# Performance work log

Measured on AMD Instinct MI355X. Metric: run time of the kernel, lower is better.

Reference implementation:

```python
import jax, jax.numpy as jnp
import numpy as np
from jax import lax

B, N, C = 32, 4096, 512
HEADS, K, U = 4, 16, 4
V = C // HEADS  # 128
KS = 7
EPS = 1e-3  # keras LayerNormalization default epsilon


def _layernorm(x, g, b):
    mu = jnp.mean(x, axis=-1, keepdims=True)
    var = jnp.var(x, axis=-1, keepdims=True)
    return (x - mu) * lax.rsqrt(var + EPS) * g + b


def setup_inputs() -> dict:
    key = jax.random.key(0)
    ks = jax.random.split(key, 6)
    sc = lambda fan: 1.0 / np.sqrt(fan)
    x = jax.random.normal(ks[0], (B, N, C), dtype=jnp.float32)
    wq = jax.random.normal(ks[1], (C, K * HEADS), dtype=jnp.float32) * sc(C)
    wk = jax.random.normal(ks[2], (C, K * U), dtype=jnp.float32) * sc(C)
    wv = jax.random.normal(ks[3], (C, V * U), dtype=jnp.float32) * sc(C)
    gq = jnp.ones((K * HEADS,), jnp.float32)
    bq = jnp.zeros((K * HEADS,), jnp.float32)
    gv = jnp.ones((V * U,), jnp.float32)
    bv = jnp.zeros((V * U,), jnp.float32)
    pos_w = jax.random.normal(ks[4], (1, KS, U, K), dtype=jnp.float32) * sc(KS * U)
    pos_b = jnp.zeros((K,), jnp.float32)
    return {"x": x, "wq": wq, "wk": wk, "wv": wv, "gq": gq, "bq": bq,
            "gv": gv, "bv": bv, "pos_w": pos_w, "pos_b": pos_b}


def reference(x, wq, wk, wv, gq, bq, gv, bv, pos_w, pos_b):
    # 1x1 conv projections == per-position matmuls
    q = _layernorm(x @ wq, gq, bq)                      # (B, N, K*HEADS)
    k = x @ wk                                          # (B, N, K*U)
    v = _layernorm(x @ wv, gv, bv)                      # (B, N, V*U)
    # rearranges (Reshape + Permute((2,3,1)))
    q = q.reshape(B, N, HEADS, K).transpose(0, 2, 3, 1)  # (B, H, K, N)
    k = k.reshape(B, N, U, K).transpose(0, 2, 3, 1)      # (B, U, K, N)
    v = v.reshape(B, N, U, V).transpose(0, 2, 3, 1)      # (B, U, V, N)
    k = jax.nn.softmax(k, axis=-1)                       # softmax over positions n
    # content lambda
    lc = jnp.einsum('bukn,buvn->bkv', k, v)              # (B, K, V)
    yc = jnp.einsum('bhkn,bkv->bnhv', q, lc)             # (B, N, H, V)
    # positional lambda: Conv2D(K, (1, KS), 'same') over (B, V, N, U) NHWC
    v2 = v.transpose(0, 2, 3, 1)                         # (B, V, N, U)
    lp = lax.conv_general_dilated(v2, pos_w, (1, 1), 'SAME',
                                  dimension_numbers=('NHWC', 'HWIO', 'NHWC')) + pos_b  # (B, V, N, K)
    lp = lp.transpose(0, 1, 3, 2)                        # (B, V, K, N)
    yp = jnp.einsum('bhkn,bvkn->bnhv', q, lp)            # (B, N, H, V)
    return (yc + yp).reshape(B, N, HEADS * V)            # (B, N, out_dim)
```

## Files before the change

### kernel.cpp

```cpp
#include <hip/hip_runtime.h>
#include <hip/hip_bf16.h>


#define Bb   32
#define Nn   4096
#define Cc   512
#define Hh   4
#define Kk   16
#define Uu   4
#define Vv   128
#define QKVW 640
#define EPSf 1e-3f

typedef __bf16 bf16;
typedef bf16  bf16x8 __attribute__((ext_vector_type(8)));
typedef bf16  bf16x4 __attribute__((ext_vector_type(4)));
typedef float f32x4  __attribute__((ext_vector_type(4)));

#define WT_OFF   0UL
#define QKV_OFF  655360UL
#define QMU_OFF  168427520UL
#define QRS_OFF  168951808UL
#define VMU_OFF  169476096UL
#define VRS_OFF  170000384UL
#define KPM_OFF  170524672UL
#define KPS_OFF  170590208UL
#define KMX_OFF  170655744UL
#define KIV_OFF  170663936UL
#define LCP_OFF  170672128UL
#define LC_OFF   174866432UL

__device__ inline float bf2f(bf16 x) { return (float)x; }

__global__ __launch_bounds__(256) void k0_weights(
    const float* __restrict__ wq, const float* __restrict__ wk,
    const float* __restrict__ wv, bf16* __restrict__ wt)
{
    int idx = blockIdx.x * 256 + threadIdx.x;
    if (idx >= Cc * QKVW) return;
    int c = idx / QKVW, j = idx % QKVW;
    float v;
    if (j < 64)       v = wq[c * 64 + j];
    else if (j < 128) v = wk[c * 64 + (j - 64)];
    else              v = wv[c * 512 + (j - 128)];
    wt[(size_t)j * Cc + c] = (bf16)v;
}

__global__ __launch_bounds__(256) void k1_gemm(
    const float* __restrict__ x, const bf16* __restrict__ wt,
    bf16* __restrict__ qkv)
{
    int bid = blockIdx.x;
    int swz = (bid & 7) * 640 + (bid >> 3);
    int bm = swz / 5, bn = swz % 5;
    int row0 = bm * 128, col0 = bn * 128;

    int tid  = threadIdx.x;
    int lane = tid & 63, w = tid >> 6;
    int wr = (w >> 1) * 64, wc = (w & 1) * 64;
    int l15 = lane & 15, l4 = lane >> 4;

    __shared__ __align__(16) bf16 As[128 * 72];
    __shared__ __align__(16) bf16 Bs[128 * 72];

    f32x4 acc[4][4];
#pragma unroll
    for (int m = 0; m < 4; ++m)
#pragma unroll
        for (int c = 0; c < 4; ++c) { acc[m][c][0]=0.f; acc[m][c][1]=0.f; acc[m][c][2]=0.f; acc[m][c][3]=0.f; }

    const int srow = tid >> 3;
    const int schk = (tid & 7) * 8;

    for (int kt = 0; kt < 8; ++kt) {
        int kb = kt * 64;
        __syncthreads();
#pragma unroll
        for (int it = 0; it < 4; ++it) {
            int r = it * 32 + srow;
            const float* src = x + (size_t)(row0 + r) * Cc + kb + schk;
            f32x4 lo = *(const f32x4*)src;
            f32x4 hi = *(const f32x4*)(src + 4);
            bf16x8 pk;
            pk[0]=(bf16)lo[0]; pk[1]=(bf16)lo[1]; pk[2]=(bf16)lo[2]; pk[3]=(bf16)lo[3];
            pk[4]=(bf16)hi[0]; pk[5]=(bf16)hi[1]; pk[6]=(bf16)hi[2]; pk[7]=(bf16)hi[3];
            *(bf16x8*)&As[r * 72 + schk] = pk;
        }
#pragma unroll
        for (int it = 0; it < 4; ++it) {
            int cI = it * 32 + srow;
            bf16x8 bvv = *(const bf16x8*)(wt + (size_t)(col0 + cI) * Cc + kb + schk);
            *(bf16x8*)&Bs[cI * 72 + schk] = bvv;
        }
        __syncthreads();
#pragma unroll
        for (int kk = 0; kk < 2; ++kk) {
            int ko = kk * 32 + l4 * 8;
            bf16x8 aF[4], bF[4];
#pragma unroll
            for (int m = 0; m < 4; ++m)
                aF[m] = *(const bf16x8*)&As[(wr + 16 * m + l15) * 72 + ko];
#pragma unroll
            for (int c = 0; c < 4; ++c)
                bF[c] = *(const bf16x8*)&Bs[(wc + 16 * c + l15) * 72 + ko];
#pragma unroll
            for (int m = 0; m < 4; ++m)
#pragma unroll
                for (int c = 0; c < 4; ++c)
                    acc[m][c] = __builtin_amdgcn_mfma_f32_16x16x32_bf16(aF[m], bF[c], acc[m][c], 0, 0, 0);
        }
    }
#pragma unroll
    for (int m = 0; m < 4; ++m)
#pragma unroll
        for (int c = 0; c < 4; ++c) {
            int grow = row0 + wr + 16 * m + l4 * 4;
            int gcol = col0 + wc + 16 * c + l15;
#pragma unroll
            for (int r = 0; r < 4; ++r)
                qkv[(size_t)(grow + r) * QKVW + gcol] = (bf16)acc[m][c][r];
        }
}

__global__ __launch_bounds__(256) void k2a_kpart(
    const bf16* __restrict__ qkv, float* __restrict__ kpm, float* __restrict__ kps)
{
    int ns = blockIdx.x;
    int b  = blockIdx.y;
    int t  = threadIdx.x;
    int c0 = (t & 7) * 8;
    int stripe = t >> 3;
    float m[8], s[8];
#pragma unroll
    for (int j = 0; j < 8; ++j) { m[j] = -1e30f; s[j] = 0.f; }
    for (int i = 0; i < 16; ++i) {
        int n = ns * 512 + stripe + i * 32;
        bf16x8 kv = *(const bf16x8*)(qkv + (size_t)(b * Nn + n) * QKVW + 64 + c0);
#pragma unroll
        for (int j = 0; j < 8; ++j) {
            float f = bf2f(kv[j]);
            float mn = fmaxf(m[j], f);
            s[j] = s[j] * __expf(m[j] - mn) + __expf(f - mn);
            m[j] = mn;
        }
    }
    __shared__ float pm[64 * 32], ps[64 * 32];
#pragma unroll
    for (int j = 0; j < 8; ++j) { pm[(c0 + j) * 32 + stripe] = m[j]; ps[(c0 + j) * 32 + stripe] = s[j]; }
    __syncthreads();
    if (t < 64) {
        float M = -1e30f;
        for (int i = 0; i < 32; ++i) M = fmaxf(M, pm[t * 32 + i]);
        float S = 0.f;
        for (int i = 0; i < 32; ++i) S += ps[t * 32 + i] * __expf(pm[t * 32 + i] - M);
        kpm[(b * 8 + ns) * 64 + t] = M;
        kps[(b * 8 + ns) * 64 + t] = S;
    }
}

__global__ __launch_bounds__(256) void k2a2_kfinal(
    const float* __restrict__ kpm, const float* __restrict__ kps,
    float* __restrict__ kmax, float* __restrict__ kinv)
{
    int idx = blockIdx.x * 256 + threadIdx.x;
    if (idx >= 2048) return;
    int b = idx >> 6, c = idx & 63;
    float M = -1e30f;
#pragma unroll
    for (int ns = 0; ns < 8; ++ns) M = fmaxf(M, kpm[(b * 8 + ns) * 64 + c]);
    float S = 0.f;
#pragma unroll
    for (int ns = 0; ns < 8; ++ns) S += kps[(b * 8 + ns) * 64 + c] * __expf(kpm[(b * 8 + ns) * 64 + c] - M);
    kmax[idx] = M;
    kinv[idx] = 1.0f / S;
}

__global__ __launch_bounds__(256) void k2b_lnstats(
    const bf16* __restrict__ qkv, float* __restrict__ qmu, float* __restrict__ qrs,
    float* __restrict__ vmu, float* __restrict__ vrs)
{
    int row = blockIdx.x * 256 + threadIdx.x;
    const bf16* p = qkv + (size_t)row * QKVW;
    float s = 0.f, ss = 0.f;
#pragma unroll
    for (int i = 0; i < 8; ++i) {
        bf16x8 v = *(const bf16x8*)(p + i * 8);
#pragma unroll
        for (int j = 0; j < 8; ++j) { float f = bf2f(v[j]); s += f; ss += f * f; }
    }
    float mu = s * (1.f / 64.f);
    float var = ss * (1.f / 64.f) - mu * mu;
    qmu[row] = mu; qrs[row] = rsqrtf(var + EPSf);
    s = 0.f; ss = 0.f;
#pragma unroll
    for (int i = 0; i < 64; ++i) {
        bf16x8 v = *(const bf16x8*)(p + 128 + i * 8);
#pragma unroll
        for (int j = 0; j < 8; ++j) { float f = bf2f(v[j]); s += f; ss += f * f; }
    }
    mu = s * (1.f / 512.f);
    var = ss * (1.f / 512.f) - mu * mu;
    vmu[row] = mu; vrs[row] = rsqrtf(var + EPSf);
}

__global__ __launch_bounds__(256) void k3_lc(
    const bf16* __restrict__ qkv, const float* __restrict__ kmax, const float* __restrict__ kinv,
    const float* __restrict__ vmu, const float* __restrict__ vrs,
    const float* __restrict__ gv, const float* __restrict__ bv,
    float* __restrict__ lcp)
{
    int ns = blockIdx.x;
    int b  = blockIdx.y;
    int t  = threadIdx.x;

    __shared__ __align__(16) float vln[16 * 512];
    __shared__ float smk[16 * 64];
    __shared__ float gvl[512], bvl[512];
    for (int i = t; i < 512; i += 256) { gvl[i] = gv[i]; bvl[i] = bv[i]; }

    int kk = t >> 4, vg = t & 15;
    float acc[8];
#pragma unroll
    for (int j = 0; j < 8; ++j) acc[j] = 0.f;

    for (int ch = 0; ch < 16; ++ch) {
        int nb = ns * 256 + ch * 16;
        __syncthreads();
        {
            int c0  = (t & 63) * 8;
            int nl0 = t >> 6;
#pragma unroll
            for (int i = 0; i < 4; ++i) {
                int nl = nl0 + i * 4;
                int row = b * Nn + nb + nl;
                bf16x8 v8 = *(const bf16x8*)(qkv + (size_t)row * QKVW + 128 + c0);
                float mu = vmu[row], rs = vrs[row];
#pragma unroll
                for (int j = 0; j < 8; ++j)
                    vln[nl * 512 + c0 + j] = (bf2f(v8[j]) - mu) * rs * gvl[c0 + j] + bvl[c0 + j];
            }
        }
        {
            int c0 = (t & 15) * 4;
            int nl = t >> 4;
            int row = b * Nn + nb + nl;
            bf16x4 k4 = *(const bf16x4*)(qkv + (size_t)row * QKVW + 64 + c0);
#pragma unroll
            for (int j = 0; j < 4; ++j)
                smk[nl * 64 + c0 + j] = __expf(bf2f(k4[j]) - kmax[b * 64 + c0 + j]) * kinv[b * 64 + c0 + j];
        }
        __syncthreads();
#pragma unroll 4
        for (int nl = 0; nl < 16; ++nl) {
#pragma unroll
            for (int u = 0; u < 4; ++u) {
                float sm = smk[nl * 64 + u * 16 + kk];
                f32x4 a = *(const f32x4*)&vln[nl * 512 + u * 128 + vg * 8];
                f32x4 c = *(const f32x4*)&vln[nl * 512 + u * 128 + vg * 8 + 4];
                acc[0] += sm * a[0]; acc[1] += sm * a[1]; acc[2] += sm * a[2]; acc[3] += sm * a[3];
                acc[4] += sm * c[0]; acc[5] += sm * c[1]; acc[6] += sm * c[2]; acc[7] += sm * c[3];
            }
        }
    }
    float* dst = lcp + (size_t)(b * 16 + ns) * 2048 + kk * 128 + vg * 8;
#pragma unroll
    for (int j = 0; j < 8; ++j) dst[j] = acc[j];
}

__global__ __launch_bounds__(256) void k3b_lcreduce(
    const float* __restrict__ lcp, float* __restrict__ lc)
{
    int idx = blockIdx.x * 256 + threadIdx.x;
    int b = idx >> 11, cc = idx & 2047;
    float s = 0.f;
#pragma unroll
    for (int ns = 0; ns < 16; ++ns) s += lcp[(size_t)(b * 16 + ns) * 2048 + cc];
    lc[idx] = s;
}

#define TN4    16
#define NPAN4  15
#define PELEM  1056

__global__ __launch_bounds__(256) void k4_out(
    const bf16* __restrict__ qkv, const float* __restrict__ qmu, const float* __restrict__ qrs,
    const float* __restrict__ vmu, const float* __restrict__ vrs,
    const float* __restrict__ gq, const float* __restrict__ bq,
    const float* __restrict__ gv, const float* __restrict__ bv,
    const float* __restrict__ posw, const float* __restrict__ posb,
    const float* __restrict__ lc, float* __restrict__ out)
{
    const int nt = blockIdx.x, b = blockIdx.y, t = threadIdx.x;
    const int n0 = nt * TN4;

    __shared__ __align__(16) bf16 PN[NPAN4 * PELEM];
    __shared__ __align__(16) bf16 Ax[64 * 104];
    __shared__ __align__(16) bf16 PP[4 * 256];

    bf16x8 z8;
#pragma unroll
    for (int j = 0; j < 8; ++j) z8[j] = (bf16)0.f;
    for (int i = t; i < 832; i += 256) *(bf16x8*)&Ax[i * 8] = z8;
    if (t < 128) *(bf16x8*)&PP[t * 8] = z8;
    __syncthreads();

    if (t < 64) {
        int g = t >> 5, du = t & 31;
        if (du < 28) {
            f32x4 a = *(const f32x4*)(posw + du * 16 + g * 8);
            f32x4 c = *(const f32x4*)(posw + du * 16 + g * 8 + 4);
            bf16x8 pk;
            pk[0]=(bf16)a[0]; pk[1]=(bf16)a[1]; pk[2]=(bf16)a[2]; pk[3]=(bf16)a[3];
            pk[4]=(bf16)c[0]; pk[5]=(bf16)c[1]; pk[6]=(bf16)c[2]; pk[7]=(bf16)c[3];
            *(bf16x8*)&PP[g * 256 + du * 8] = pk;
        }
    }
    {
        int p = t >> 7, v = t & 127;
        const float* src = lc + b * 2048 + p * 8 * 128 + v;
        bf16x8 pk;
#pragma unroll
        for (int j = 0; j < 8; ++j) pk[j] = (bf16)src[j * 128];
        *(bf16x8*)&PN[p * PELEM + v * 8] = pk;
        if (t < 128) {
            bf16x8 ones = z8; ones[0] = (bf16)1.0f;
            *(bf16x8*)&PN[2 * PELEM + t * 8] = ones;
            *(bf16x8*)&PN[3 * PELEM + t * 8] = z8;
        }
    }
    for (int it = t; it < 22 * 16; it += 256) {
        int lr = it >> 4, vo = it & 15;
        int n  = n0 - 3 + lr;
        int pbase = (4 + (lr >> 1)) * PELEM + (lr & 1) * 4;
        if ((unsigned)n < (unsigned)Nn) {
            int row = b * Nn + n;
            float mu = vmu[row], rs = vrs[row];
            float f[4][8];
#pragma unroll
            for (int u = 0; u < 4; ++u) {
                bf16x8 v8 = *(const bf16x8*)(qkv + (size_t)row * QKVW + 128 + u * 128 + vo * 8);
                f32x4 g0 = *(const f32x4*)(gv + u * 128 + vo * 8);
                f32x4 g1 = *(const f32x4*)(gv + u * 128 + vo * 8 + 4);
                f32x4 b0 = *(const f32x4*)(bv + u * 128 + vo * 8);
                f32x4 b1 = *(const f32x4*)(bv + u * 128 + vo * 8 + 4);
#pragma unroll
                for (int j = 0; j < 4; ++j) f[u][j]     = (bf2f(v8[j])     - mu) * rs * g0[j] + b0[j];
#pragma unroll
                for (int j = 0; j < 4; ++j) f[u][4 + j] = (bf2f(v8[4 + j]) - mu) * rs * g1[j] + b1[j];
            }
#pragma unroll
            for (int vi = 0; vi < 8; ++vi) {
                bf16x4 pk;
                pk[0]=(bf16)f[0][vi]; pk[1]=(bf16)f[1][vi]; pk[2]=(bf16)f[2][vi]; pk[3]=(bf16)f[3][vi];
                *(bf16x4*)&PN[pbase + (vo * 8 + vi) * 8] = pk;
            }
        } else {
            bf16x4 zz; zz[0]=(bf16)0.f; zz[1]=(bf16)0.f; zz[2]=(bf16)0.f; zz[3]=(bf16)0.f;
#pragma unroll
            for (int vi = 0; vi < 8; ++vi)
                *(bf16x4*)&PN[pbase + (vo * 8 + vi) * 8] = zz;
        }
    }
    if (t < 128) {
        int row = t >> 1, half = t & 1;
        int n = n0 + (row >> 2), h = row & 3;
        int gr = b * Nn + n;
        int c0 = h * 16 + half * 8;
        bf16x8 q8 = *(const bf16x8*)(qkv + (size_t)gr * QKVW + c0);
        float mu = qmu[gr], rs = qrs[gr];
        f32x4 gg0 = *(const f32x4*)(gq + c0), gg1 = *(const f32x4*)(gq + c0 + 4);
        f32x4 bb0 = *(const f32x4*)(bq + c0), bb1 = *(const f32x4*)(bq + c0 + 4);
        f32x4 pb0 = *(const f32x4*)(posb + half * 8), pb1 = *(const f32x4*)(posb + half * 8 + 4);
        float qbp = 0.f;
        bf16x8 pk;
#pragma unroll
        for (int j = 0; j < 4; ++j) {
            float f = (bf2f(q8[j]) - mu) * rs * gg0[j] + bb0[j];
            qbp += f * pb0[j]; pk[j] = (bf16)f;
        }
#pragma unroll
        for (int j = 0; j < 4; ++j) {
            float f = (bf2f(q8[4 + j]) - mu) * rs * gg1[j] + bb1[j];
            qbp += f * pb1[j]; pk[4 + j] = (bf16)f;
        }
        *(bf16x8*)&Ax[row * 104 + half * 8] = pk;
        float qb = qbp + __shfl_xor(qbp, 1);
        if (!half) Ax[row * 104 + 16] = (bf16)qb;
    }
    __syncthreads();

    const int lane = t & 63, rt = t >> 6;
    const int g = lane >> 4, l15 = lane & 15;
    const int arow = rt * 16 + l15;

    bf16x8 aF0 = *(const bf16x8*)&Ax[arow * 104 + g * 8];
    f32x4 zf; zf[0]=0.f; zf[1]=0.f; zf[2]=0.f; zf[3]=0.f;
#pragma unroll
    for (int ct = 0; ct < 2; ++ct) {
        bf16x8 bp = *(const bf16x8*)&PP[g * 256 + (ct * 16 + l15) * 8];
        f32x4 rf = __builtin_amdgcn_mfma_f32_16x16x32_bf16(aF0, bp, zf, 0, 0, 0);
        int du = ct * 16 + l15;
#pragma unroll
        for (int reg = 0; reg < 4; ++reg) {
            int row = rt * 16 + g * 4 + reg;
            Ax[row * 104 + 32 + g * 4 + du] = (bf16)rf[reg];
        }
    }

    bf16x8 aF1 = *(const bf16x8*)&Ax[arow * 104 + 32 + g * 8];
    bf16x8 aF2 = *(const bf16x8*)&Ax[arow * 104 + 64 + g * 8];
    const int P1 = (4 + rt * 2 + g) * PELEM;
    const int P2 = (4 + rt * 2 + 4) * PELEM;
    f32x4 acc[8];
#pragma unroll
    for (int c = 0; c < 8; ++c) acc[c] = zf;
#pragma unroll
    for (int c = 0; c < 8; ++c) {
        int vb = (c * 16 + l15) * 8;
        bf16x8 b0 = *(const bf16x8*)&PN[g * PELEM + vb];
        bf16x8 b1 = *(const bf16x8*)&PN[P1 + vb];
        bf16x8 b2 = *(const bf16x8*)&PN[P2 + vb];
        acc[c] = __builtin_amdgcn_mfma_f32_16x16x32_bf16(aF0, b0, acc[c], 0, 0, 0);
        acc[c] = __builtin_amdgcn_mfma_f32_16x16x32_bf16(aF1, b1, acc[c], 0, 0, 0);
        acc[c] = __builtin_amdgcn_mfma_f32_16x16x32_bf16(aF2, b2, acc[c], 0, 0, 0);
    }
#pragma unroll
    for (int c = 0; c < 8; ++c) {
#pragma unroll
        for (int reg = 0; reg < 4; ++reg) {
            int row = rt * 16 + g * 4 + reg;
            int n = n0 + (row >> 2), h = row & 3;
            out[((size_t)(b * Nn + n)) * 512 + h * 128 + c * 16 + l15] = acc[c][reg];
        }
    }
}

extern "C" void kernel_launch(void* const* d_in, const int* in_sizes, int n_in,
                              void* d_out, int out_size, void* d_ws, size_t ws_size,
                              hipStream_t stream) {
    const float* x    = (const float*)d_in[0];
    const float* wq   = (const float*)d_in[1];
    const float* wk   = (const float*)d_in[2];
    const float* wv   = (const float*)d_in[3];
    const float* gq   = (const float*)d_in[4];
    const float* bq   = (const float*)d_in[5];
    const float* gv   = (const float*)d_in[6];
    const float* bv   = (const float*)d_in[7];
    const float* posw = (const float*)d_in[8];
    const float* posb = (const float*)d_in[9];
    float* out = (float*)d_out;

    char* ws = (char*)d_ws;
    bf16*  wt   = (bf16*)(ws + WT_OFF);
    bf16*  qkv  = (bf16*)(ws + QKV_OFF);
    float* qmu  = (float*)(ws + QMU_OFF);
    float* qrs  = (float*)(ws + QRS_OFF);
    float* vmu  = (float*)(ws + VMU_OFF);
    float* vrs  = (float*)(ws + VRS_OFF);
    float* kpm  = (float*)(ws + KPM_OFF);
    float* kps  = (float*)(ws + KPS_OFF);
    float* kmax = (float*)(ws + KMX_OFF);
    float* kinv = (float*)(ws + KIV_OFF);
    float* lcp  = (float*)(ws + LCP_OFF);
    float* lc   = (float*)(ws + LC_OFF);

    k0_weights<<<(Cc * QKVW + 255) / 256, 256, 0, stream>>>(wq, wk, wv, wt);
    k1_gemm<<<5120, 256, 0, stream>>>(x, wt, qkv);
    k2a_kpart<<<dim3(8, 32), 256, 0, stream>>>(qkv, kpm, kps);
    k2a2_kfinal<<<8, 256, 0, stream>>>(kpm, kps, kmax, kinv);
    k2b_lnstats<<<512, 256, 0, stream>>>(qkv, qmu, qrs, vmu, vrs);
    k3_lc<<<dim3(16, 32), 256, 0, stream>>>(qkv, kmax, kinv, vmu, vrs, gv, bv, lcp);
    k3b_lcreduce<<<256, 256, 0, stream>>>(lcp, lc);
    k4_out<<<dim3(Nn / TN4, Bb), 256, 0, stream>>>(qkv, qmu, qrs, vmu, vrs, gq, bq, gv, bv,
                                                   posw, posb, lc, out);
}
```

Before: 438.7 us.

## Prefetch A tile into registers, load B via direct-to-LDS, XOR-swizzle shared tiles

The projection GEMM now prefetches the next fp32 x tile into registers while the current tile is used, so global load latency overlaps with compute. The weight tile is loaded straight into LDS with global_load_lds instead of passing through registers. Both shared tiles drop the padded stride of 72 for an XOR-swizzled stride of 64 to avoid bank conflicts. This raises register pressure and relies on the direct-to-LDS layout matching the swizzled read pattern.

```diff
diff --git a/kernel.cpp b/kernel.cpp
--- a/kernel.cpp
+++ b/kernel.cpp
@@ -58,10 +58,10 @@
     int tid  = threadIdx.x;
     int lane = tid & 63, w = tid >> 6;
     int wr = (w >> 1) * 64, wc = (w & 1) * 64;
-    int l15 = lane & 15, l4 = lane >> 4;
-
-    __shared__ __align__(16) bf16 As[128 * 72];
-    __shared__ __align__(16) bf16 Bs[128 * 72];
+    int l15 = lane & 15, g = lane >> 4;
+
+    __shared__ __align__(16) bf16 As[128 * 64];
+    __shared__ __align__(16) bf16 Bs[128 * 64];
 
     f32x4 acc[4][4];
 #pragma unroll
@@ -69,40 +69,65 @@
 #pragma unroll
         for (int c = 0; c < 4; ++c) { acc[m][c][0]=0.f; acc[m][c][1]=0.f; acc[m][c][2]=0.f; acc[m][c][3]=0.f; }
 
-    const int srow = tid >> 3;
-    const int schk = (tid & 7) * 8;
+    const int ar  = tid >> 3;
+    const int as  = tid & 7;
+    const int asw = ((as ^ (ar & 7)) * 8);
+    const float* aptr = x + (size_t)(row0 + ar) * Cc + as * 8;
+
+    const int brl = lane >> 3;
+    const int bsl = lane & 7;
+
+    f32x4 pA[4][2];
+#pragma unroll
+    for (int it = 0; it < 4; ++it) {
+        const float* src = aptr + (size_t)it * 32 * Cc;
+        pA[it][0] = *(const f32x4*)src;
+        pA[it][1] = *(const f32x4*)(src + 4);
+    }
 
     for (int kt = 0; kt < 8; ++kt) {
-        int kb = kt * 64;
+        const int kb = kt * 64;
         __syncthreads();
 #pragma unroll
         for (int it = 0; it < 4; ++it) {
-            int r = it * 32 + srow;
-            const float* src = x + (size_t)(row0 + r) * Cc + kb + schk;
-            f32x4 lo = *(const f32x4*)src;
-            f32x4 hi = *(const f32x4*)(src + 4);
+            int r = it * 32 + ar;
             bf16x8 pk;
-            pk[0]=(bf16)lo[0]; pk[1]=(bf16)lo[1]; pk[2]=(bf16)lo[2]; pk[3]=(bf16)lo[3];
-            pk[4]=(bf16)hi[0]; pk[5]=(bf16)hi[1]; pk[6]=(bf16)hi[2]; pk[7]=(bf16)hi[3];
-            *(bf16x8*)&As[r * 72 + schk] = pk;
-        }
-#pragma unroll
-        for (int it = 0; it < 4; ++it) {
-            int cI = it * 32 + srow;
-            bf16x8 bvv = *(const bf16x8*)(wt + (size_t)(col0 + cI) * Cc + kb + schk);
-            *(bf16x8*)&Bs[cI * 72 + schk] = bvv;
+            pk[0]=(bf16)pA[it][0][0]; pk[1]=(bf16)pA[it][0][1];
+            pk[2]=(bf16)pA[it][0][2]; pk[3]=(bf16)pA[it][0][3];
+            pk[4]=(bf16)pA[it][1][0]; pk[5]=(bf16)pA[it][1][1];
+            pk[6]=(bf16)pA[it][1][2]; pk[7]=(bf16)pA[it][1][3];
+            *(bf16x8*)&As[r * 64 + asw] = pk;
+        }
+#pragma unroll
+        for (int i = 0; i < 4; ++i) {
+            int grp = w * 4 + i;
+            int row = grp * 8 + brl;
+            const bf16* src = wt + (size_t)(col0 + row) * Cc + kb + ((bsl ^ (row & 7)) * 8);
+            __builtin_amdgcn_global_load_lds((const void*)src,
+                                             (void*)((char*)Bs + grp * 1024), 16, 0, 0);
+        }
+        if (kt < 7) {
+#pragma unroll
+            for (int it = 0; it < 4; ++it) {
+                const float* src = aptr + (size_t)it * 32 * Cc + (kb + 64);
+                pA[it][0] = *(const f32x4*)src;
+                pA[it][1] = *(const f32x4*)(src + 4);
+            }
         }
         __syncthreads();
 #pragma unroll
         for (int kk = 0; kk < 2; ++kk) {
-            int ko = kk * 32 + l4 * 8;
             bf16x8 aF[4], bF[4];
 #pragma unroll
-            for (int m = 0; m < 4; ++m)
-                aF[m] = *(const bf16x8*)&As[(wr + 16 * m + l15) * 72 + ko];
-#pragma unroll
-            for (int c = 0; c < 4; ++c)
-                bF[c] = *(const bf16x8*)&Bs[(wc + 16 * c + l15) * 72 + ko];
+            for (int m = 0; m < 4; ++m) {
+                int r = wr + 16 * m + l15;
+                aF[m] = *(const bf16x8*)&As[r * 64 + (((kk * 4 + g) ^ (r & 7)) * 8)];
+            }
+#pragma unroll
+            for (int c = 0; c < 4; ++c) {
+                int r = wc + 16 * c + l15;
+                bF[c] = *(const bf16x8*)&Bs[r * 64 + (((kk * 4 + g) ^ (r & 7)) * 8)];
+            }
 #pragma unroll
             for (int m = 0; m < 4; ++m)
 #pragma unroll
@@ -114,7 +139,7 @@
     for (int m = 0; m < 4; ++m)
 #pragma unroll
         for (int c = 0; c < 4; ++c) {
-            int grow = row0 + wr + 16 * m + l4 * 4;
+            int grow = row0 + wr + 16 * m + (lane >> 4) * 4;
             int gcol = col0 + wc + 16 * c + l15;
 #pragma unroll
             for (int r = 0; r < 4; ++r)
```

Result: slower. 460.7 us (+5.0%).

## Double-buffer GEMM B tile via async global-to-LDS loads, load A directly to registers

Applied to the files above, without the earlier changes.

The projection GEMM no longer stages the fp32 activation tile through shared memory. Each wave loads its A fragments straight from global into registers and converts them to bf16 there. The weight tile is double-buffered in LDS with XOR-swizzled layout using global_load_lds, with manual vmcnt waits and barriers so the next tile's loads overlap the current MFMA work. Separately, the key-softmax partial pass gets twice as many blocks (16 stripes per batch) for more parallelism, and its scratch is relocated into the lcp region. Risks include the hand-counted vmcnt values and redundant A loads across the two column waves.

```diff
diff --git a/kernel.cpp b/kernel.cpp
--- a/kernel.cpp
+++ b/kernel.cpp
@@ -23,8 +23,6 @@
 #define QRS_OFF  168951808UL
 #define VMU_OFF  169476096UL
 #define VRS_OFF  170000384UL
-#define KPM_OFF  170524672UL
-#define KPS_OFF  170590208UL
 #define KMX_OFF  170655744UL
 #define KIV_OFF  170663936UL
 #define LCP_OFF  170672128UL
@@ -46,7 +44,7 @@
     wt[(size_t)j * Cc + c] = (bf16)v;
 }
 
-__global__ __launch_bounds__(256) void k1_gemm(
+__global__ __launch_bounds__(256) void k1_gemm_fast(
     const float* __restrict__ x, const bf16* __restrict__ wt,
     bf16* __restrict__ qkv)
 {
@@ -58,10 +56,9 @@
     int tid  = threadIdx.x;
     int lane = tid & 63, w = tid >> 6;
     int wr = (w >> 1) * 64, wc = (w & 1) * 64;
-    int l15 = lane & 15, l4 = lane >> 4;
-
-    __shared__ __align__(16) bf16 As[128 * 72];
-    __shared__ __align__(16) bf16 Bs[128 * 72];
+    int l15 = lane & 15, g = lane >> 4;
+
+    __shared__ __align__(16) bf16 Bs[2][128 * 64];
 
     f32x4 acc[4][4];
 #pragma unroll
@@ -69,52 +66,72 @@
 #pragma unroll
         for (int c = 0; c < 4; ++c) { acc[m][c][0]=0.f; acc[m][c][1]=0.f; acc[m][c][2]=0.f; acc[m][c][3]=0.f; }
 
-    const int srow = tid >> 3;
-    const int schk = (tid & 7) * 8;
+    const int srow = lane >> 3;
+    const int ssl  = lane & 7;
+    const int sslw = (ssl ^ srow) * 8;
+    const bf16* bBase = wt + (size_t)(col0 + srow) * Cc + sslw;
+
+    auto stageB = [&](int buf, int kb) {
+#pragma unroll
+        for (int i = 0; i < 4; ++i) {
+            int grp = w * 4 + i;
+            __builtin_amdgcn_global_load_lds(
+                (const void*)(bBase + (size_t)grp * 8 * Cc + kb),
+                (void*)((char*)&Bs[buf][0] + grp * 1024), 16, 0, 0);
+        }
+    };
+
+    const float* aBase = x + (size_t)(row0 + wr + l15) * Cc + g * 8;
+
+    stageB(0, 0);
 
     for (int kt = 0; kt < 8; ++kt) {
-        int kb = kt * 64;
-        __syncthreads();
-#pragma unroll
-        for (int it = 0; it < 4; ++it) {
-            int r = it * 32 + srow;
-            const float* src = x + (size_t)(row0 + r) * Cc + kb + schk;
-            f32x4 lo = *(const f32x4*)src;
-            f32x4 hi = *(const f32x4*)(src + 4);
-            bf16x8 pk;
-            pk[0]=(bf16)lo[0]; pk[1]=(bf16)lo[1]; pk[2]=(bf16)lo[2]; pk[3]=(bf16)lo[3];
-            pk[4]=(bf16)hi[0]; pk[5]=(bf16)hi[1]; pk[6]=(bf16)hi[2]; pk[7]=(bf16)hi[3];
-            *(bf16x8*)&As[r * 72 + schk] = pk;
-        }
-#pragma unroll
-        for (int it = 0; it < 4; ++it) {
-            int cI = it * 32 + srow;
-            bf16x8 bvv = *(const bf16x8*)(wt + (size_t)(col0 + cI) * Cc + kb + schk);
-            *(bf16x8*)&Bs[cI * 72 + schk] = bvv;
-        }
-        __syncthreads();
+        const int cur = kt & 1;
+        f32x4 pA[4][2][2];
+#pragma unroll
+        for (int m = 0; m < 4; ++m) {
+            const float* pm = aBase + (size_t)(16 * m) * Cc + kt * 64;
+            pA[m][0][0] = *(const f32x4*)(pm);
+            pA[m][0][1] = *(const f32x4*)(pm + 4);
+            pA[m][1][0] = *(const f32x4*)(pm + 32);
+            pA[m][1][1] = *(const f32x4*)(pm + 36);
+        }
+        if (kt < 7) {
+            stageB(cur ^ 1, (kt + 1) * 64);
+            asm volatile("s_waitcnt vmcnt(20)\n\ts_barrier" ::: "memory");
+        } else {
+            asm volatile("s_waitcnt vmcnt(16)\n\ts_barrier" ::: "memory");
+        }
 #pragma unroll
         for (int kk = 0; kk < 2; ++kk) {
-            int ko = kk * 32 + l4 * 8;
             bf16x8 aF[4], bF[4];
 #pragma unroll
-            for (int m = 0; m < 4; ++m)
-                aF[m] = *(const bf16x8*)&As[(wr + 16 * m + l15) * 72 + ko];
-#pragma unroll
-            for (int c = 0; c < 4; ++c)
-                bF[c] = *(const bf16x8*)&Bs[(wc + 16 * c + l15) * 72 + ko];
+            for (int m = 0; m < 4; ++m) {
+                bf16x8 pk;
+                pk[0]=(bf16)pA[m][kk][0][0]; pk[1]=(bf16)pA[m][kk][0][1];
+                pk[2]=(bf16)pA[m][kk][0][2]; pk[3]=(bf16)pA[m][kk][0][3];
+                pk[4]=(bf16)pA[m][kk][1][0]; pk[5]=(bf16)pA[m][kk][1][1];
+                pk[6]=(bf16)pA[m][kk][1][2]; pk[7]=(bf16)pA[m][kk][1][3];
+                aF[m] = pk;
+            }
+#pragma unroll
+            for (int c = 0; c < 4; ++c) {
+                int r = wc + 16 * c + l15;
+                bF[c] = *(const bf16x8*)&Bs[cur][r * 64 + (((kk * 4 + g) ^ (r & 7)) * 8)];
+            }
 #pragma unroll
             for (int m = 0; m < 4; ++m)
 #pragma unroll
                 for (int c = 0; c < 4; ++c)
                     acc[m][c] = __builtin_amdgcn_mfma_f32_16x16x32_bf16(aF[m], bF[c], acc[m][c], 0, 0, 0);
         }
+        if (kt < 7) asm volatile("s_barrier" ::: "memory");
     }
 #pragma unroll
     for (int m = 0; m < 4; ++m)
 #pragma unroll
         for (int c = 0; c < 4; ++c) {
-            int grow = row0 + wr + 16 * m + l4 * 4;
+            int grow = row0 + wr + 16 * m + g * 4;
             int gcol = col0 + wc + 16 * c + l15;
 #pragma unroll
             for (int r = 0; r < 4; ++r)
@@ -133,8 +150,8 @@
     float m[8], s[8];
 #pragma unroll
     for (int j = 0; j < 8; ++j) { m[j] = -1e30f; s[j] = 0.f; }
-    for (int i = 0; i < 16; ++i) {
-        int n = ns * 512 + stripe + i * 32;
+    for (int i = 0; i < 8; ++i) {
+        int n = ns * 256 + stripe + i * 32;
         bf16x8 kv = *(const bf16x8*)(qkv + (size_t)(b * Nn + n) * QKVW + 64 + c0);
 #pragma unroll
         for (int j = 0; j < 8; ++j) {
@@ -153,8 +170,8 @@
         for (int i = 0; i < 32; ++i) M = fmaxf(M, pm[t * 32 + i]);
         float S = 0.f;
         for (int i = 0; i < 32; ++i) S += ps[t * 32 + i] * __expf(pm[t * 32 + i] - M);
-        kpm[(b * 8 + ns) * 64 + t] = M;
-        kps[(b * 8 + ns) * 64 + t] = S;
+        kpm[(b * 16 + ns) * 64 + t] = M;
+        kps[(b * 16 + ns) * 64 + t] = S;
     }
 }
 
@@ -167,10 +184,10 @@
     int b = idx >> 6, c = idx & 63;
     float M = -1e30f;
 #pragma unroll
-    for (int ns = 0; ns < 8; ++ns) M = fmaxf(M, kpm[(b * 8 + ns) * 64 + c]);
+    for (int ns = 0; ns < 16; ++ns) M = fmaxf(M, kpm[(b * 16 + ns) * 64 + c]);
     float S = 0.f;
 #pragma unroll
-    for (int ns = 0; ns < 8; ++ns) S += kps[(b * 8 + ns) * 64 + c] * __expf(kpm[(b * 8 + ns) * 64 + c] - M);
+    for (int ns = 0; ns < 16; ++ns) S += kps[(b * 16 + ns) * 64 + c] * __expf(kpm[(b * 16 + ns) * 64 + c] - M);
     kmax[idx] = M;
     kinv[idx] = 1.0f / S;
 }
@@ -457,16 +474,16 @@
     float* qrs  = (float*)(ws + QRS_OFF);
     float* vmu  = (float*)(ws + VMU_OFF);
     float* vrs  = (float*)(ws + VRS_OFF);
-    float* kpm  = (float*)(ws + KPM_OFF);
-    float* kps  = (float*)(ws + KPS_OFF);
     float* kmax = (float*)(ws + KMX_OFF);
     float* kinv = (float*)(ws + KIV_OFF);
     float* lcp  = (float*)(ws + LCP_OFF);
     float* lc   = (float*)(ws + LC_OFF);
+    float* kpm  = (float*)(ws + LCP_OFF);
+    float* kps  = (float*)(ws + LCP_OFF + 131072);
 
     k0_weights<<<(Cc * QKVW + 255) / 256, 256, 0, stream>>>(wq, wk, wv, wt);
-    k1_gemm<<<5120, 256, 0, stream>>>(x, wt, qkv);
-    k2a_kpart<<<dim3(8, 32), 256, 0, stream>>>(qkv, kpm, kps);
+    k1_gemm_fast<<<5120, 256, 0, stream>>>(x, wt, qkv);
+    k2a_kpart<<<dim3(16, 32), 256, 0, stream>>>(qkv, kpm, kps);
     k2a2_kfinal<<<8, 256, 0, stream>>>(kpm, kps, kmax, kinv);
     k2b_lnstats<<<512, 256, 0, stream>>>(qkv, qmu, qrs, vmu, vrs);
     k3_lc<<<dim3(16, 32), 256, 0, stream>>>(qkv, kmax, kinv, vmu, vrs, gv, bv, lcp);
```

After: 608.8 us. +38.8%, slower.
